# Kernel tuning notes

Hardware: AMD Instinct MI355X
Metric: run time of the kernel (lower is better)

The kernel has to match this reference:

```python
import jax, jax.numpy as jnp
import numpy as np

N = 100_000   # atoms
B = 10_000    # building blocks
E = 320_000   # edges (bb <- atom)
D = 256       # embed_dim
H = 8         # heads
HD = D // H   # head_dim = 32
DIST = 64     # gaussian dist embed dim
MAX_R = 10.0


def setup_inputs() -> dict:
    key = jax.random.key(0)
    ks = jax.random.split(key, 10)
    atom_feats = jax.random.normal(ks[0], (N, D), jnp.float32)
    coords = jax.random.normal(ks[1], (N, 3), jnp.float32) * 3.0
    bb_vec = jnp.sort(jax.random.randint(ks[2], (N,), 0, B, jnp.int32))
    src = jax.random.randint(ks[3], (E,), 0, N, jnp.int32)
    tgt = jax.random.randint(ks[4], (E,), 0, B, jnp.int32)
    # linear params, [in, out] layout (x @ W + b)
    Wq = jax.random.normal(ks[5], (D, D), jnp.float32) / np.sqrt(D)
    Wk = jax.random.normal(ks[6], (D + DIST, D), jnp.float32) / np.sqrt(D + DIST)
    Wv = jax.random.normal(ks[7], (D + DIST, D), jnp.float32) / np.sqrt(D + DIST)
    Wo = jax.random.normal(ks[8], (D, D), jnp.float32) / np.sqrt(D)
    bq = jnp.zeros((D,), jnp.float32)
    bk = jnp.zeros((D,), jnp.float32)
    bv = jnp.zeros((D,), jnp.float32)
    bo = jnp.zeros((D,), jnp.float32)
    return dict(atom_feats=atom_feats, coords=coords, Wq=Wq, bq=bq, Wk=Wk, bk=bk,
                Wv=Wv, bv=bv, Wo=Wo, bo=bo, bb_vec=bb_vec, src=src, tgt=tgt)


def _gaussian_smearing(dist):
    offsets = jnp.linspace(0.0, MAX_R, DIST)            # [DIST]
    coeff = -0.5 / (offsets[1] - offsets[0]) ** 2
    return jnp.exp(coeff * (dist[:, None] - offsets) ** 2)  # [E, DIST]


def reference(atom_feats, coords, Wq, bq, Wk, bk, Wv, bv, Wo, bo, bb_vec, src, tgt):
    # building-block centers: mean coords, summed feats per bb
    counts = jax.ops.segment_sum(jnp.ones((N,), coords.dtype), bb_vec, num_segments=B)
    bb_center_pos = jax.ops.segment_sum(coords, bb_vec, num_segments=B)
    bb_center_pos = bb_center_pos / jnp.maximum(counts, 1.0)[:, None]       # [B, 3]
    bb_center_feats = jax.ops.segment_sum(atom_feats, bb_vec, num_segments=B)  # [B, D]

    # per-edge distance embedding
    edge_vec = coords[src] - bb_center_pos[tgt]                             # [E, 3]
    dist = jnp.sqrt(jnp.sum(edge_vec * edge_vec, axis=-1))                  # [E]
    edge_dist_embed = _gaussian_smearing(dist)                              # [E, DIST]

    # QKV
    q = (bb_center_feats @ Wq + bq).reshape(B, H, HD)                       # [B, H, HD]
    atom_input = jnp.concatenate([atom_feats[src], edge_dist_embed], -1)    # [E, D+DIST]
    k = (atom_input @ Wk + bk).reshape(E, H, HD)
    v = (atom_input @ Wv + bv).reshape(E, H, HD)

    # per-edge attention logits + segment softmax over tgt
    attn = jnp.einsum('ehc,ehc->eh', q[tgt], k) / np.sqrt(HD)               # [E, H]
    seg_max = jax.ops.segment_max(attn, tgt, num_segments=B)                # [B, H]
    ex = jnp.exp(attn - seg_max[tgt])
    denom = jax.ops.segment_sum(ex, tgt, num_segments=B)                    # [B, H]
    attn = ex / (denom[tgt] + 1e-16)

    # weighted scatter-sum of messages
    msg = attn[..., None] * v                                               # [E, H, HD]
    out = jax.ops.segment_sum(msg, tgt, num_segments=B).reshape(B, D)       # [B, D]
    return out @ Wo + bo
```

## Files before the change

### kernel.cpp

```cpp
#include <hip/hip_runtime.h>
#include <math.h>

#define N_ATOMS 100000
#define B_BB    10000
#define E_EDGES 320000
#define D_DIM   256
#define NHEAD   8
#define NDIST   64
#define EPAD    128

#define DELTA   (10.0f/63.0f)
#define GCOEFF  (-0.5f/(DELTA*DELTA))
#define QKSCALE 0.17677669529663687f

__global__ void k_offsets(const int* __restrict__ bb_vec, int* __restrict__ atom_off,
                          int* __restrict__ edge_cnt) {
  int b = blockIdx.x * 256 + threadIdx.x;
  if (b <= B_BB) {
    int lo = 0, hi = N_ATOMS;
    while (lo < hi) { int mid = (lo + hi) >> 1; if (bb_vec[mid] < b) lo = mid + 1; else hi = mid; }
    atom_off[b] = lo;
  }
  if (b < B_BB) edge_cnt[b] = 0;
}

__global__ __launch_bounds__(256) void k_bb_centers(
    const float* __restrict__ af, const float* __restrict__ coords,
    const int* __restrict__ atom_off, float* __restrict__ bbF, float* __restrict__ bb_pos) {
  int t = threadIdx.x;
  for (int b = blockIdx.x; b < B_BB; b += gridDim.x) {
    int s = atom_off[b], e = atom_off[b + 1];
    float acc = 0.f;
    for (int a = s; a < e; a++) acc += af[(size_t)a * D_DIM + t];
    bbF[(size_t)b * D_DIM + t] = acc;
    if (t < 3) {
      float c = 0.f;
      for (int a = s; a < e; a++) c += coords[(size_t)a * 3 + t];
      float cnt = (float)(e - s);
      bb_pos[b * 4 + t] = c / fmaxf(cnt, 1.0f);
    }
  }
}

__global__ __launch_bounds__(256) void k_gemm256(
    const float* __restrict__ A, const float* __restrict__ W,
    const float* __restrict__ bias, float* __restrict__ C, int M) {
  __shared__ __align__(16) float As[16][68];
  __shared__ __align__(16) float Ws[16][64];
  int tid = threadIdx.x;
  int tx = tid & 15, ty = tid >> 4;
  int row0 = blockIdx.x * 64, col0 = blockIdx.y * 64;
  float acc[4][4] = {};
  for (int k0 = 0; k0 < 256; k0 += 16) {
    {
      int r = tid >> 2;
      int c = (tid & 3) * 4;
      int row = row0 + r;
      float4 v = make_float4(0.f, 0.f, 0.f, 0.f);
      if (row < M) v = *(const float4*)&A[(size_t)row * 256 + k0 + c];
      As[c + 0][r] = v.x; As[c + 1][r] = v.y; As[c + 2][r] = v.z; As[c + 3][r] = v.w;
    }
    {
      int r = tid >> 4;
      int c = (tid & 15) * 4;
      float4 v = *(const float4*)&W[(size_t)(k0 + r) * 256 + col0 + c];
      *(float4*)&Ws[r][c] = v;
    }
    __syncthreads();
#pragma unroll
    for (int kk = 0; kk < 16; kk++) {
      float4 a = *(const float4*)&As[kk][ty * 4];
      float4 b = *(const float4*)&Ws[kk][tx * 4];
      float av[4] = {a.x, a.y, a.z, a.w};
      float bv4[4] = {b.x, b.y, b.z, b.w};
#pragma unroll
      for (int i = 0; i < 4; i++)
#pragma unroll
        for (int j = 0; j < 4; j++) acc[i][j] += av[i] * bv4[j];
    }
    __syncthreads();
  }
#pragma unroll
  for (int i = 0; i < 4; i++) {
    int row = row0 + ty * 4 + i;
    if (row < M) {
      int col = col0 + tx * 4;
      float4 r = make_float4(acc[i][0] + bias[col + 0], acc[i][1] + bias[col + 1],
                             acc[i][2] + bias[col + 2], acc[i][3] + bias[col + 3]);
      *(float4*)&C[(size_t)row * 256 + col] = r;
    }
  }
}

__global__ void k_hist(const int* __restrict__ tgt, int* __restrict__ edge_cnt) {
  int e = blockIdx.x * 256 + threadIdx.x;
  if (e < E_EDGES) atomicAdd(&edge_cnt[tgt[e]], 1);
}

__global__ __launch_bounds__(1024) void k_scan(
    const int* __restrict__ edge_cnt, int* __restrict__ edge_start, int* __restrict__ cursor,
    int* __restrict__ src_sorted, float* __restrict__ dist_sorted) {
  __shared__ int ssum[1024];
  int tid = threadIdx.x;
  int base = tid * 10;
  int v[10]; int s = 0;
#pragma unroll
  for (int k = 0; k < 10; k++) { int i = base + k; v[k] = (i < B_BB) ? edge_cnt[i] : 0; s += v[k]; }
  ssum[tid] = s;
  __syncthreads();
  for (int off = 1; off < 1024; off <<= 1) {
    int t = (tid >= off) ? ssum[tid - off] : 0;
    __syncthreads();
    ssum[tid] += t;
    __syncthreads();
  }
  int excl = ssum[tid] - s;
#pragma unroll
  for (int k = 0; k < 10; k++) {
    int i = base + k;
    if (i < B_BB) { edge_start[i] = excl; cursor[i] = excl; }
    excl += v[k];
  }
  if (tid == 1023) edge_start[B_BB] = E_EDGES;
  if (tid < EPAD) { src_sorted[E_EDGES + tid] = 0; dist_sorted[E_EDGES + tid] = 0.f; }
}

__global__ void k_fill(const int* __restrict__ src, const int* __restrict__ tgt,
                       const float* __restrict__ coords, const float* __restrict__ bb_pos,
                       int* __restrict__ cursor, int* __restrict__ src_sorted,
                       float* __restrict__ dist_sorted) {
  int e = blockIdx.x * 256 + threadIdx.x;
  if (e >= E_EDGES) return;
  int b = tgt[e], a = src[e];
  int pos = atomicAdd(&cursor[b], 1);
  float dx = coords[a * 3 + 0] - bb_pos[b * 4 + 0];
  float dy = coords[a * 3 + 1] - bb_pos[b * 4 + 1];
  float dz = coords[a * 3 + 2] - bb_pos[b * 4 + 2];
  src_sorted[pos] = a;
  dist_sorted[pos] = sqrtf(dx * dx + dy * dy + dz * dz);
}

__global__ __launch_bounds__(256) void k_wt(
    const float* __restrict__ q, const float* __restrict__ Wk, float* __restrict__ wt) {
  __shared__ __align__(16) float As[32][132];
  __shared__ __align__(16) float Bs[32][68];
  int tid = threadIdx.x;
  int b0 = blockIdx.x * 128;
  int i0 = blockIdx.y * 64;
  int h  = blockIdx.z;
  {
    int r = tid >> 1, c0 = (tid & 1) * 16;
    int row = b0 + r;
    const float* qp = q + (size_t)row * 256 + h * 32 + c0;
#pragma unroll
    for (int jj = 0; jj < 4; ++jj) {
      float4 v = make_float4(0.f, 0.f, 0.f, 0.f);
      if (row < B_BB) v = *(const float4*)(qp + 4 * jj);
      As[c0 + 4*jj + 0][r] = v.x; As[c0 + 4*jj + 1][r] = v.y;
      As[c0 + 4*jj + 2][r] = v.z; As[c0 + 4*jj + 3][r] = v.w;
    }
  }
  {
    int r = tid >> 2, c0 = (tid & 3) * 8;
    const float* wp = Wk + (size_t)(i0 + r) * 256 + h * 32 + c0;
#pragma unroll
    for (int jj = 0; jj < 2; ++jj) {
      float4 v = *(const float4*)(wp + 4 * jj);
      Bs[c0 + 4*jj + 0][r] = v.x; Bs[c0 + 4*jj + 1][r] = v.y;
      Bs[c0 + 4*jj + 2][r] = v.z; Bs[c0 + 4*jj + 3][r] = v.w;
    }
  }
  __syncthreads();
  int tx = tid & 15, ty = tid >> 4;
  float acc[8][4] = {};
#pragma unroll
  for (int kk = 0; kk < 32; ++kk) {
    float4 a0 = *(const float4*)&As[kk][ty * 8];
    float4 a1 = *(const float4*)&As[kk][ty * 8 + 4];
    float4 b4 = *(const float4*)&Bs[kk][tx * 4];
    float av[8] = {a0.x, a0.y, a0.z, a0.w, a1.x, a1.y, a1.z, a1.w};
    float bv4[4] = {b4.x, b4.y, b4.z, b4.w};
#pragma unroll
    for (int i = 0; i < 8; ++i)
#pragma unroll
      for (int j = 0; j < 4; ++j) acc[i][j] += av[i] * bv4[j];
  }
#pragma unroll
  for (int i = 0; i < 8; ++i) {
    int row = b0 + ty * 8 + i;
    if (row < B_BB) {
      float4 o = make_float4(acc[i][0] * QKSCALE, acc[i][1] * QKSCALE,
                             acc[i][2] * QKSCALE, acc[i][3] * QKSCALE);
      *(float4*)&wt[(size_t)row * 2560 + h * 320 + i0 + tx * 4] = o;
    }
  }
}

#define FMA4(p, v, Wb, k) \
  p = fmaf((v).x, Wb[(k)], p);   p = fmaf((v).y, Wb[(k)+1], p); \
  p = fmaf((v).z, Wb[(k)+2], p); p = fmaf((v).w, Wb[(k)+3], p);

#define ACC4(Sarr, k, ww, v) \
  Sarr[(k)]   = fmaf(ww, (v).x, Sarr[(k)]);   Sarr[(k)+1] = fmaf(ww, (v).y, Sarr[(k)+1]); \
  Sarr[(k)+2] = fmaf(ww, (v).z, Sarr[(k)+2]); Sarr[(k)+3] = fmaf(ww, (v).w, Sarr[(k)+3]);

__global__ __launch_bounds__(256) void k_attn(
    const float* __restrict__ af, float* __restrict__ wtS,
    const int* __restrict__ edge_start, const int* __restrict__ src_sorted,
    const float* __restrict__ dist_sorted, float* __restrict__ wsum) {
  int tid = threadIdx.x;
  int lane = tid & 63;
  int wv = tid >> 6;
  int h0 = 2 * wv, h1 = 2 * wv + 1;
  int g = lane >> 4;
  int sub = lane & 15;
  int b = blockIdx.x;

  int s0 = edge_start[b], e1 = edge_start[b + 1];
  float* wtb = wtS + (size_t)b * 2560;
  const float* wr0 = wtb + h0 * 320;
  const float* wr1 = wtb + h1 * 320;

  float W0[16], W1[16], wd0[4], wd1[4];
#pragma unroll
  for (int j = 0; j < 4; ++j) {
    float4 t0 = *(const float4*)(wr0 + sub * 16 + 4 * j);
    float4 t1 = *(const float4*)(wr1 + sub * 16 + 4 * j);
    W0[4*j+0] = t0.x; W0[4*j+1] = t0.y; W0[4*j+2] = t0.z; W0[4*j+3] = t0.w;
    W1[4*j+0] = t1.x; W1[4*j+1] = t1.y; W1[4*j+2] = t1.z; W1[4*j+3] = t1.w;
  }
#pragma unroll
  for (int j = 0; j < 4; ++j) { wd0[j] = wr0[256 + sub + 16*j]; wd1[j] = wr1[256 + sub + 16*j]; }

  float cj[4];
#pragma unroll
  for (int j = 0; j < 4; ++j) cj[j] = (float)(sub + 16 * j) * DELTA;

  float l0 = 0.f, l1 = 0.f;
  float S0r[16] = {}, S1r[16] = {};
  float sd0[4] = {}, sd1[4] = {};

  if (s0 < e1) {
    int iaC = src_sorted[s0 + 8 + g];
    int iaD = src_sorted[s0 + 12 + g];
    float ddA = dist_sorted[s0 + g];
    float ddB = dist_sorted[s0 + 4 + g];
    float ddC = dist_sorted[s0 + 8 + g];
    float ddD = dist_sorted[s0 + 12 + g];
    int iaA = src_sorted[s0 + g];
    int iaB = src_sorted[s0 + 4 + g];
    const float4* rA = (const float4*)(af + (size_t)iaA * 256 + sub * 16);
    const float4* rB = (const float4*)(af + (size_t)iaB * 256 + sub * 16);
    float4 A0 = rA[0], A1 = rA[1], A2 = rA[2], A3 = rA[3];
    float4 B0 = rB[0], B1 = rB[1], B2 = rB[2], B3 = rB[3];

    for (int eb = s0; eb < e1; eb += 8) {
      int iaC2 = src_sorted[eb + 16 + g];
      float ddC2 = dist_sorted[eb + 16 + g];
      int iaD2 = src_sorted[eb + 20 + g];
      float ddD2 = dist_sorted[eb + 20 + g];
      const float4* rC = (const float4*)(af + (size_t)iaC * 256 + sub * 16);
      float4 C0 = rC[0], C1 = rC[1], C2 = rC[2], C3 = rC[3];

      float embA[4], embB[4];
#pragma unroll
      for (int j = 0; j < 4; ++j) {
        float da = ddA - cj[j]; embA[j] = __expf(GCOEFF * da * da);
        float db = ddB - cj[j]; embB[j] = __expf(GCOEFF * db * db);
      }
      float pA0 = 0.f, pA1 = 0.f, pB0 = 0.f, pB1 = 0.f;
      FMA4(pA0, A0, W0, 0);  FMA4(pA1, A0, W1, 0);
      FMA4(pB0, B0, W0, 0);  FMA4(pB1, B0, W1, 0);
      FMA4(pA0, A1, W0, 4);  FMA4(pA1, A1, W1, 4);
      FMA4(pB0, B1, W0, 4);  FMA4(pB1, B1, W1, 4);
      FMA4(pA0, A2, W0, 8);  FMA4(pA1, A2, W1, 8);
      FMA4(pB0, B2, W0, 8);  FMA4(pB1, B2, W1, 8);
      FMA4(pA0, A3, W0, 12); FMA4(pA1, A3, W1, 12);
      FMA4(pB0, B3, W0, 12); FMA4(pB1, B3, W1, 12);
#pragma unroll
      for (int j = 0; j < 4; ++j) {
        pA0 = fmaf(embA[j], wd0[j], pA0); pA1 = fmaf(embA[j], wd1[j], pA1);
        pB0 = fmaf(embB[j], wd0[j], pB0); pB1 = fmaf(embB[j], wd1[j], pB1);
      }
#pragma unroll
      for (int off = 8; off > 0; off >>= 1) {
        pA0 += __shfl_xor(pA0, off);
        pA1 += __shfl_xor(pA1, off);
        pB0 += __shfl_xor(pB0, off);
        pB1 += __shfl_xor(pB1, off);
      }
      float wA0 = __expf(pA0), wA1 = __expf(pA1);
      float wB0 = __expf(pB0), wB1 = __expf(pB1);
      if (eb + g >= e1)     { wA0 = 0.f; wA1 = 0.f; }
      if (eb + 4 + g >= e1) { wB0 = 0.f; wB1 = 0.f; }
      l0 += wA0 + wB0; l1 += wA1 + wB1;
#pragma unroll
      for (int j = 0; j < 4; ++j) {
        sd0[j] = fmaf(wA0, embA[j], sd0[j]); sd1[j] = fmaf(wA1, embA[j], sd1[j]);
        sd0[j] = fmaf(wB0, embB[j], sd0[j]); sd1[j] = fmaf(wB1, embB[j], sd1[j]);
      }

      ACC4(S0r, 0,  wA0, A0); ACC4(S1r, 0,  wA1, A0);
      ACC4(S0r, 4,  wA0, A1); ACC4(S1r, 4,  wA1, A1);
      ACC4(S0r, 8,  wA0, A2); ACC4(S1r, 8,  wA1, A2);
      ACC4(S0r, 12, wA0, A3); ACC4(S1r, 12, wA1, A3);

      const float4* rD = (const float4*)(af + (size_t)iaD * 256 + sub * 16);
      float4 D0 = rD[0], D1 = rD[1], D2 = rD[2], D3 = rD[3];

      ACC4(S0r, 0,  wB0, B0); ACC4(S1r, 0,  wB1, B0);
      ACC4(S0r, 4,  wB0, B1); ACC4(S1r, 4,  wB1, B1);
      ACC4(S0r, 8,  wB0, B2); ACC4(S1r, 8,  wB1, B2);
      ACC4(S0r, 12, wB0, B3); ACC4(S1r, 12, wB1, B3);

      A0 = C0; A1 = C1; A2 = C2; A3 = C3;
      B0 = D0; B1 = D1; B2 = D2; B3 = D3;
      ddA = ddC; ddB = ddD; ddC = ddC2; ddD = ddD2;
      iaC = iaC2; iaD = iaD2;
    }
  }

#pragma unroll
  for (int off = 16; off <= 32; off <<= 1) {
    l0 += __shfl_xor(l0, off);
    l1 += __shfl_xor(l1, off);
#pragma unroll
    for (int c = 0; c < 16; ++c) {
      S0r[c] += __shfl_xor(S0r[c], off);
      S1r[c] += __shfl_xor(S1r[c], off);
    }
#pragma unroll
    for (int j = 0; j < 4; ++j) {
      sd0[j] += __shfl_xor(sd0[j], off);
      sd1[j] += __shfl_xor(sd1[j], off);
    }
  }

  float inv0 = 1.0f / (l0 + 1e-16f), inv1 = 1.0f / (l1 + 1e-16f);
  if (g == 0) {
#pragma unroll
    for (int j = 0; j < 4; ++j) {
      float4 o0 = make_float4(S0r[4*j+0]*inv0, S0r[4*j+1]*inv0, S0r[4*j+2]*inv0, S0r[4*j+3]*inv0);
      float4 o1 = make_float4(S1r[4*j+0]*inv1, S1r[4*j+1]*inv1, S1r[4*j+2]*inv1, S1r[4*j+3]*inv1);
      *(float4*)(wtb + h0 * 320 + sub * 16 + 4 * j) = o0;
      *(float4*)(wtb + h1 * 320 + sub * 16 + 4 * j) = o1;
    }
#pragma unroll
    for (int j = 0; j < 4; ++j) {
      wtb[h0 * 320 + 256 + sub + 16 * j] = sd0[j] * inv0;
      wtb[h1 * 320 + 256 + sub + 16 * j] = sd1[j] * inv1;
    }
    if (sub == 0) {
      wsum[b * 8 + h0] = l0 * inv0;
      wsum[b * 8 + h1] = l1 * inv1;
    }
  }
}

__global__ __launch_bounds__(256) void k_out_head(
    const float* __restrict__ Sf, const float* __restrict__ Wv,
    const float* __restrict__ bv, const float* __restrict__ wsum,
    float* __restrict__ out_pre) {
  __shared__ __align__(16) float As[32][132];
  __shared__ __align__(16) float Bs[32][36];
  int tid = threadIdx.x;
  int b0 = blockIdx.x * 128;
  int h  = blockIdx.y;
  int tx = tid & 7, ty = tid >> 3;
  float acc[4][4] = {};
  for (int k0 = 0; k0 < 320; k0 += 32) {
    {
      int r = tid >> 1, c0 = (tid & 1) * 16;
      int row = b0 + r;
      const float* sp = Sf + (size_t)row * 2560 + h * 320 + k0 + c0;
#pragma unroll
      for (int jj = 0; jj < 4; ++jj) {
        float4 v = make_float4(0.f, 0.f, 0.f, 0.f);
        if (row < B_BB) v = *(const float4*)(sp + 4 * jj);
        As[c0 + 4*jj + 0][r] = v.x; As[c0 + 4*jj + 1][r] = v.y;
        As[c0 + 4*jj + 2][r] = v.z; As[c0 + 4*jj + 3][r] = v.w;
      }
    }
    {
      int r = tid >> 3, c0 = (tid & 7) * 4;
      float4 v = *(const float4*)&Wv[(size_t)(k0 + r) * 256 + h * 32 + c0];
      *(float4*)&Bs[r][c0] = v;
    }
    __syncthreads();
#pragma unroll
    for (int kk = 0; kk < 32; ++kk) {
      float4 a4 = *(const float4*)&As[kk][ty * 4];
      float4 b4 = *(const float4*)&Bs[kk][tx * 4];
      float av[4] = {a4.x, a4.y, a4.z, a4.w};
      float bv4[4] = {b4.x, b4.y, b4.z, b4.w};
#pragma unroll
      for (int i = 0; i < 4; ++i)
#pragma unroll
        for (int j = 0; j < 4; ++j) acc[i][j] += av[i] * bv4[j];
    }
    __syncthreads();
  }
  float bvv[4];
#pragma unroll
  for (int j = 0; j < 4; ++j) bvv[j] = bv[h * 32 + tx * 4 + j];
#pragma unroll
  for (int i = 0; i < 4; ++i) {
    int row = b0 + ty * 4 + i;
    if (row < B_BB) {
      float ws = wsum[row * 8 + h];
      float4 o = make_float4(acc[i][0] + ws * bvv[0], acc[i][1] + ws * bvv[1],
                             acc[i][2] + ws * bvv[2], acc[i][3] + ws * bvv[3]);
      *(float4*)&out_pre[(size_t)row * 256 + h * 32 + tx * 4] = o;
    }
  }
}

extern "C" void kernel_launch(void* const* d_in, const int* in_sizes, int n_in,
                              void* d_out, int out_size, void* d_ws, size_t ws_size,
                              hipStream_t stream) {
  const float* af     = (const float*)d_in[0];
  const float* coords = (const float*)d_in[1];
  const float* Wq     = (const float*)d_in[2];
  const float* bq     = (const float*)d_in[3];
  const float* Wk     = (const float*)d_in[4];
  const float* bk     = (const float*)d_in[5];  (void)bk;
  const float* Wv     = (const float*)d_in[6];
  const float* bv     = (const float*)d_in[7];
  const float* Wo     = (const float*)d_in[8];
  const float* bo     = (const float*)d_in[9];
  const int* bb_vec   = (const int*)d_in[10];
  const int* src      = (const int*)d_in[11];
  const int* tgt      = (const int*)d_in[12];
  float* out = (float*)d_out;
  (void)in_sizes; (void)n_in; (void)out_size; (void)ws_size;

  char* ws = (char*)d_ws;
  size_t o = 0;
  auto alloc = [&](size_t bytes) { size_t r = o; o += (bytes + 255) & ~(size_t)255; return r; };
  int*   atom_off    = (int*)(ws + alloc((B_BB + 1) * 4));
  int*   edge_cnt    = (int*)(ws + alloc((size_t)B_BB * 4));
  int*   edge_start  = (int*)(ws + alloc((B_BB + 1) * 4));
  int*   cursor      = (int*)(ws + alloc((size_t)B_BB * 4));
  int*   src_sorted  = (int*)(ws + alloc((size_t)(E_EDGES + EPAD) * 4));
  float* dist_sorted = (float*)(ws + alloc((size_t)(E_EDGES + EPAD) * 4));
  float* bbF         = (float*)(ws + alloc((size_t)B_BB * 256 * 4));
  float* bb_pos      = (float*)(ws + alloc((size_t)B_BB * 4 * 4));
  float* q           = (float*)(ws + alloc((size_t)B_BB * 256 * 4));
  float* wtS         = (float*)(ws + alloc((size_t)B_BB * 2560 * 4));
  float* wsum        = (float*)(ws + alloc((size_t)B_BB * 8 * 4));
  float* out_pre     = (float*)(ws + alloc((size_t)B_BB * 256 * 4));

  k_offsets<<<(B_BB + 1 + 255) / 256, 256, 0, stream>>>(bb_vec, atom_off, edge_cnt);
  k_bb_centers<<<2560, 256, 0, stream>>>(af, coords, atom_off, bbF, bb_pos);
  k_hist<<<(E_EDGES + 255) / 256, 256, 0, stream>>>(tgt, edge_cnt);
  k_scan<<<1, 1024, 0, stream>>>(edge_cnt, edge_start, cursor, src_sorted, dist_sorted);
  k_fill<<<(E_EDGES + 255) / 256, 256, 0, stream>>>(src, tgt, coords, bb_pos, cursor,
                                                    src_sorted, dist_sorted);
  k_gemm256<<<dim3((B_BB + 63) / 64, 4), 256, 0, stream>>>(bbF, Wq, bq, q, B_BB);
  k_wt<<<dim3((B_BB + 127) / 128, 5, 8), 256, 0, stream>>>(q, Wk, wtS);
  k_attn<<<B_BB, 256, 0, stream>>>(af, wtS, edge_start, src_sorted, dist_sorted, wsum);
  k_out_head<<<dim3((B_BB + 127) / 128, 8), 256, 0, stream>>>(wtS, Wv, bv, wsum, out_pre);
  k_gemm256<<<dim3((B_BB + 63) / 64, 4), 256, 0, stream>>>(out_pre, Wo, bo, out, B_BB);
}
```

Baseline: 557.7 us.

## Double-buffer shared tiles in gemm256 and process several blocks per attention workgroup

The 256-wide GEMM now uses ping-pong shared-memory tiles. The next K-slice is loaded into registers while the current slice is computed, which removes one barrier per iteration and hides global load latency. The attention kernel now loops over four building blocks per workgroup instead of launching one workgroup per block. This cuts launch and scheduling overhead but reduces the grid to 2500 workgroups, which can leave more load imbalance across CUs since per-block edge counts vary.

```diff
diff --git a/kernel.cpp b/kernel.cpp
--- a/kernel.cpp
+++ b/kernel.cpp
@@ -8,6 +8,7 @@
 #define NHEAD   8
 #define NDIST   64
 #define EPAD    128
+#define BB_PER_BLK 4
 
 #define DELTA   (10.0f/63.0f)
 #define GCOEFF  (-0.5f/(DELTA*DELTA))
@@ -45,32 +46,38 @@
 __global__ __launch_bounds__(256) void k_gemm256(
     const float* __restrict__ A, const float* __restrict__ W,
     const float* __restrict__ bias, float* __restrict__ C, int M) {
-  __shared__ __align__(16) float As[16][68];
-  __shared__ __align__(16) float Ws[16][64];
+  __shared__ __align__(16) float As[2][16][68];
+  __shared__ __align__(16) float Ws[2][16][64];
   int tid = threadIdx.x;
   int tx = tid & 15, ty = tid >> 4;
   int row0 = blockIdx.x * 64, col0 = blockIdx.y * 64;
+  int ar = tid >> 2, ac = (tid & 3) * 4;
+  int wr = tid >> 4, wc = (tid & 15) * 4;
+  int arow = row0 + ar;
+  const float* Ap = A + (size_t)arow * 256 + ac;
+  const float* Wp = W + (size_t)wr * 256 + col0 + wc;
   float acc[4][4] = {};
+  {
+    float4 va = make_float4(0.f, 0.f, 0.f, 0.f);
+    if (arow < M) va = *(const float4*)Ap;
+    As[0][ac + 0][ar] = va.x; As[0][ac + 1][ar] = va.y;
+    As[0][ac + 2][ar] = va.z; As[0][ac + 3][ar] = va.w;
+    *(float4*)&Ws[0][wr][wc] = *(const float4*)Wp;
+  }
+  __syncthreads();
+  int cur = 0;
   for (int k0 = 0; k0 < 256; k0 += 16) {
-    {
-      int r = tid >> 2;
-      int c = (tid & 3) * 4;
-      int row = row0 + r;
-      float4 v = make_float4(0.f, 0.f, 0.f, 0.f);
-      if (row < M) v = *(const float4*)&A[(size_t)row * 256 + k0 + c];
-      As[c + 0][r] = v.x; As[c + 1][r] = v.y; As[c + 2][r] = v.z; As[c + 3][r] = v.w;
-    }
-    {
-      int r = tid >> 4;
-      int c = (tid & 15) * 4;
-      float4 v = *(const float4*)&W[(size_t)(k0 + r) * 256 + col0 + c];
-      *(float4*)&Ws[r][c] = v;
-    }
-    __syncthreads();
+    float4 va, vw;
+    bool nxt = (k0 + 16) < 256;
+    if (nxt) {
+      va = make_float4(0.f, 0.f, 0.f, 0.f);
+      if (arow < M) va = *(const float4*)(Ap + k0 + 16);
+      vw = *(const float4*)(Wp + (size_t)(k0 + 16) * 256);
+    }
 #pragma unroll
     for (int kk = 0; kk < 16; kk++) {
-      float4 a = *(const float4*)&As[kk][ty * 4];
-      float4 b = *(const float4*)&Ws[kk][tx * 4];
+      float4 a = *(const float4*)&As[cur][kk][ty * 4];
+      float4 b = *(const float4*)&Ws[cur][kk][tx * 4];
       float av[4] = {a.x, a.y, a.z, a.w};
       float bv4[4] = {b.x, b.y, b.z, b.w};
 #pragma unroll
@@ -78,7 +85,13 @@
 #pragma unroll
         for (int j = 0; j < 4; j++) acc[i][j] += av[i] * bv4[j];
     }
-    __syncthreads();
+    if (nxt) {
+      As[cur ^ 1][ac + 0][ar] = va.x; As[cur ^ 1][ac + 1][ar] = va.y;
+      As[cur ^ 1][ac + 2][ar] = va.z; As[cur ^ 1][ac + 3][ar] = va.w;
+      *(float4*)&Ws[cur ^ 1][wr][wc] = vw;
+      __syncthreads();
+      cur ^= 1;
+    }
   }
 #pragma unroll
   for (int i = 0; i < 4; i++) {
@@ -214,145 +227,149 @@
   int h0 = 2 * wv, h1 = 2 * wv + 1;
   int g = lane >> 4;
   int sub = lane & 15;
-  int b = blockIdx.x;
-
-  int s0 = edge_start[b], e1 = edge_start[b + 1];
-  float* wtb = wtS + (size_t)b * 2560;
-  const float* wr0 = wtb + h0 * 320;
-  const float* wr1 = wtb + h1 * 320;
-
-  float W0[16], W1[16], wd0[4], wd1[4];
-#pragma unroll
-  for (int j = 0; j < 4; ++j) {
-    float4 t0 = *(const float4*)(wr0 + sub * 16 + 4 * j);
-    float4 t1 = *(const float4*)(wr1 + sub * 16 + 4 * j);
-    W0[4*j+0] = t0.x; W0[4*j+1] = t0.y; W0[4*j+2] = t0.z; W0[4*j+3] = t0.w;
-    W1[4*j+0] = t1.x; W1[4*j+1] = t1.y; W1[4*j+2] = t1.z; W1[4*j+3] = t1.w;
-  }
-#pragma unroll
-  for (int j = 0; j < 4; ++j) { wd0[j] = wr0[256 + sub + 16*j]; wd1[j] = wr1[256 + sub + 16*j]; }
 
   float cj[4];
 #pragma unroll
   for (int j = 0; j < 4; ++j) cj[j] = (float)(sub + 16 * j) * DELTA;
 
-  float l0 = 0.f, l1 = 0.f;
-  float S0r[16] = {}, S1r[16] = {};
-  float sd0[4] = {}, sd1[4] = {};
-
-  if (s0 < e1) {
-    int iaC = src_sorted[s0 + 8 + g];
-    int iaD = src_sorted[s0 + 12 + g];
-    float ddA = dist_sorted[s0 + g];
-    float ddB = dist_sorted[s0 + 4 + g];
-    float ddC = dist_sorted[s0 + 8 + g];
-    float ddD = dist_sorted[s0 + 12 + g];
-    int iaA = src_sorted[s0 + g];
-    int iaB = src_sorted[s0 + 4 + g];
-    const float4* rA = (const float4*)(af + (size_t)iaA * 256 + sub * 16);
-    const float4* rB = (const float4*)(af + (size_t)iaB * 256 + sub * 16);
-    float4 A0 = rA[0], A1 = rA[1], A2 = rA[2], A3 = rA[3];
-    float4 B0 = rB[0], B1 = rB[1], B2 = rB[2], B3 = rB[3];
-
-    for (int eb = s0; eb < e1; eb += 8) {
-      int iaC2 = src_sorted[eb + 16 + g];
-      float ddC2 = dist_sorted[eb + 16 + g];
-      int iaD2 = src_sorted[eb + 20 + g];
-      float ddD2 = dist_sorted[eb + 20 + g];
-      const float4* rC = (const float4*)(af + (size_t)iaC * 256 + sub * 16);
-      float4 C0 = rC[0], C1 = rC[1], C2 = rC[2], C3 = rC[3];
-
-      float embA[4], embB[4];
+  for (int bi = 0; bi < BB_PER_BLK; ++bi) {
+    int b = blockIdx.x * BB_PER_BLK + bi;
+    if (b >= B_BB) break;
+
+    int s0 = edge_start[b], e1 = edge_start[b + 1];
+    float* wtb = wtS + (size_t)b * 2560;
+    const float* wr0 = wtb + h0 * 320;
+    const float* wr1 = wtb + h1 * 320;
+
+    float W0[16], W1[16], wd0[4], wd1[4];
+#pragma unroll
+    for (int j = 0; j < 4; ++j) {
+      float4 t0 = *(const float4*)(wr0 + sub * 16 + 4 * j);
+      float4 t1 = *(const float4*)(wr1 + sub * 16 + 4 * j);
+      W0[4*j+0] = t0.x; W0[4*j+1] = t0.y; W0[4*j+2] = t0.z; W0[4*j+3] = t0.w;
+      W1[4*j+0] = t1.x; W1[4*j+1] = t1.y; W1[4*j+2] = t1.z; W1[4*j+3] = t1.w;
+    }
+#pragma unroll
+    for (int j = 0; j < 4; ++j) { wd0[j] = wr0[256 + sub + 16*j]; wd1[j] = wr1[256 + sub + 16*j]; }
+
+    float l0 = 0.f, l1 = 0.f;
+    float S0r[16] = {}, S1r[16] = {};
+    float sd0[4] = {}, sd1[4] = {};
+
+    if (s0 < e1) {
+      int iaC = src_sorted[s0 + 8 + g];
+      int iaD = src_sorted[s0 + 12 + g];
+      float ddA = dist_sorted[s0 + g];
+      float ddB = dist_sorted[s0 + 4 + g];
+      float ddC = dist_sorted[s0 + 8 + g];
+      float ddD = dist_sorted[s0 + 12 + g];
+      int iaA = src_sorted[s0 + g];
+      int iaB = src_sorted[s0 + 4 + g];
+      const float4* rA = (const float4*)(af + (size_t)iaA * 256 + sub * 16);
+      const float4* rB = (const float4*)(af + (size_t)iaB * 256 + sub * 16);
+      float4 A0 = rA[0], A1 = rA[1], A2 = rA[2], A3 = rA[3];
+      float4 B0 = rB[0], B1 = rB[1], B2 = rB[2], B3 = rB[3];
+
+      for (int eb = s0; eb < e1; eb += 8) {
+        int iaC2 = src_sorted[eb + 16 + g];
+        float ddC2 = dist_sorted[eb + 16 + g];
+        int iaD2 = src_sorted[eb + 20 + g];
+        float ddD2 = dist_sorted[eb + 20 + g];
+        const float4* rC = (const float4*)(af + (size_t)iaC * 256 + sub * 16);
+        float4 C0 = rC[0], C1 = rC[1], C2 = rC[2], C3 = rC[3];
+
+        float embA[4], embB[4];
+#pragma unroll
+        for (int j = 0; j < 4; ++j) {
+          float da = ddA - cj[j]; embA[j] = __expf(GCOEFF * da * da);
+          float db = ddB - cj[j]; embB[j] = __expf(GCOEFF * db * db);
+        }
+        float pA0 = 0.f, pA1 = 0.f, pB0 = 0.f, pB1 = 0.f;
+        FMA4(pA0, A0, W0, 0);  FMA4(pA1, A0, W1, 0);
+        FMA4(pB0, B0, W0, 0);  FMA4(pB1, B0, W1, 0);
+        FMA4(pA0, A1, W0, 4);  FMA4(pA1, A1, W1, 4);
+        FMA4(pB0, B1, W0, 4);  FMA4(pB1, B1, W1, 4);
+        FMA4(pA0, A2, W0, 8);  FMA4(pA1, A2, W1, 8);
+        FMA4(pB0, B2, W0, 8);  FMA4(pB1, B2, W1, 8);
+        FMA4(pA0, A3, W0, 12); FMA4(pA1, A3, W1, 12);
+        FMA4(pB0, B3, W0, 12); FMA4(pB1, B3, W1, 12);
+#pragma unroll
+        for (int j = 0; j < 4; ++j) {
+          pA0 = fmaf(embA[j], wd0[j], pA0); pA1 = fmaf(embA[j], wd1[j], pA1);
+          pB0 = fmaf(embB[j], wd0[j], pB0); pB1 = fmaf(embB[j], wd1[j], pB1);
+        }
+#pragma unroll
+        for (int off = 8; off > 0; off >>= 1) {
+          pA0 += __shfl_xor(pA0, off);
+          pA1 += __shfl_xor(pA1, off);
+          pB0 += __shfl_xor(pB0, off);
+          pB1 += __shfl_xor(pB1, off);
+        }
+        float wA0 = __expf(pA0), wA1 = __expf(pA1);
+        float wB0 = __expf(pB0), wB1 = __expf(pB1);
+        if (eb + g >= e1)     { wA0 = 0.f; wA1 = 0.f; }
+        if (eb + 4 + g >= e1) { wB0 = 0.f; wB1 = 0.f; }
+        l0 += wA0 + wB0; l1 += wA1 + wB1;
+#pragma unroll
+        for (int j = 0; j < 4; ++j) {
+          sd0[j] = fmaf(wA0, embA[j], sd0[j]); sd1[j] = fmaf(wA1, embA[j], sd1[j]);
+          sd0[j] = fmaf(wB0, embB[j], sd0[j]); sd1[j] = fmaf(wB1, embB[j], sd1[j]);
+        }
+
+        ACC4(S0r, 0,  wA0, A0); ACC4(S1r, 0,  wA1, A0);
+        ACC4(S0r, 4,  wA0, A1); ACC4(S1r, 4,  wA1, A1);
+        ACC4(S0r, 8,  wA0, A2); ACC4(S1r, 8,  wA1, A2);
+        ACC4(S0r, 12, wA0, A3); ACC4(S1r, 12, wA1, A3);
+
+        const float4* rD = (const float4*)(af + (size_t)iaD * 256 + sub * 16);
+        float4 D0 = rD[0], D1 = rD[1], D2 = rD[2], D3 = rD[3];
+
+        ACC4(S0r, 0,  wB0, B0); ACC4(S1r, 0,  wB1, B0);
+        ACC4(S0r, 4,  wB0, B1); ACC4(S1r, 4,  wB1, B1);
+        ACC4(S0r, 8,  wB0, B2); ACC4(S1r, 8,  wB1, B2);
+        ACC4(S0r, 12, wB0, B3); ACC4(S1r, 12, wB1, B3);
+
+        A0 = C0; A1 = C1; A2 = C2; A3 = C3;
+        B0 = D0; B1 = D1; B2 = D2; B3 = D3;
+        ddA = ddC; ddB = ddD; ddC = ddC2; ddD = ddD2;
+        iaC = iaC2; iaD = iaD2;
+      }
+    }
+
+#pragma unroll
+    for (int off = 16; off <= 32; off <<= 1) {
+      l0 += __shfl_xor(l0, off);
+      l1 += __shfl_xor(l1, off);
+#pragma unroll
+      for (int c = 0; c < 16; ++c) {
+        S0r[c] += __shfl_xor(S0r[c], off);
+        S1r[c] += __shfl_xor(S1r[c], off);
+      }
 #pragma unroll
       for (int j = 0; j < 4; ++j) {
-        float da = ddA - cj[j]; embA[j] = __expf(GCOEFF * da * da);
-        float db = ddB - cj[j]; embB[j] = __expf(GCOEFF * db * db);
-      }
-      float pA0 = 0.f, pA1 = 0.f, pB0 = 0.f, pB1 = 0.f;
-      FMA4(pA0, A0, W0, 0);  FMA4(pA1, A0, W1, 0);
-      FMA4(pB0, B0, W0, 0);  FMA4(pB1, B0, W1, 0);
-      FMA4(pA0, A1, W0, 4);  FMA4(pA1, A1, W1, 4);
-      FMA4(pB0, B1, W0, 4);  FMA4(pB1, B1, W1, 4);
-      FMA4(pA0, A2, W0, 8);  FMA4(pA1, A2, W1, 8);
-      FMA4(pB0, B2, W0, 8);  FMA4(pB1, B2, W1, 8);
-      FMA4(pA0, A3, W0, 12); FMA4(pA1, A3, W1, 12);
-      FMA4(pB0, B3, W0, 12); FMA4(pB1, B3, W1, 12);
+        sd0[j] += __shfl_xor(sd0[j], off);
+        sd1[j] += __shfl_xor(sd1[j], off);
+      }
+    }
+
+    float inv0 = 1.0f / (l0 + 1e-16f), inv1 = 1.0f / (l1 + 1e-16f);
+    if (g == 0) {
 #pragma unroll
       for (int j = 0; j < 4; ++j) {
-        pA0 = fmaf(embA[j], wd0[j], pA0); pA1 = fmaf(embA[j], wd1[j], pA1);
-        pB0 = fmaf(embB[j], wd0[j], pB0); pB1 = fmaf(embB[j], wd1[j], pB1);
-      }
-#pragma unroll
-      for (int off = 8; off > 0; off >>= 1) {
-        pA0 += __shfl_xor(pA0, off);
-        pA1 += __shfl_xor(pA1, off);
-        pB0 += __shfl_xor(pB0, off);
-        pB1 += __shfl_xor(pB1, off);
-      }
-      float wA0 = __expf(pA0), wA1 = __expf(pA1);
-      float wB0 = __expf(pB0), wB1 = __expf(pB1);
-      if (eb + g >= e1)     { wA0 = 0.f; wA1 = 0.f; }
-      if (eb + 4 + g >= e1) { wB0 = 0.f; wB1 = 0.f; }
-      l0 += wA0 + wB0; l1 += wA1 + wB1;
+        float4 o0 = make_float4(S0r[4*j+0]*inv0, S0r[4*j+1]*inv0, S0r[4*j+2]*inv0, S0r[4*j+3]*inv0);
+        float4 o1 = make_float4(S1r[4*j+0]*inv1, S1r[4*j+1]*inv1, S1r[4*j+2]*inv1, S1r[4*j+3]*inv1);
+        *(float4*)(wtb + h0 * 320 + sub * 16 + 4 * j) = o0;
+        *(float4*)(wtb + h1 * 320 + sub * 16 + 4 * j) = o1;
+      }
 #pragma unroll
       for (int j = 0; j < 4; ++j) {
-        sd0[j] = fmaf(wA0, embA[j], sd0[j]); sd1[j] = fmaf(wA1, embA[j], sd1[j]);
-        sd0[j] = fmaf(wB0, embB[j], sd0[j]); sd1[j] = fmaf(wB1, embB[j], sd1[j]);
-      }
-
-      ACC4(S0r, 0,  wA0, A0); ACC4(S1r, 0,  wA1, A0);
-      ACC4(S0r, 4,  wA0, A1); ACC4(S1r, 4,  wA1, A1);
-      ACC4(S0r, 8,  wA0, A2); ACC4(S1r, 8,  wA1, A2);
-      ACC4(S0r, 12, wA0, A3); ACC4(S1r, 12, wA1, A3);
-
-      const float4* rD = (const float4*)(af + (size_t)iaD * 256 + sub * 16);
-      float4 D0 = rD[0], D1 = rD[1], D2 = rD[2], D3 = rD[3];
-
-      ACC4(S0r, 0,  wB0, B0); ACC4(S1r, 0,  wB1, B0);
-      ACC4(S0r, 4,  wB0, B1); ACC4(S1r, 4,  wB1, B1);
-      ACC4(S0r, 8,  wB0, B2); ACC4(S1r, 8,  wB1, B2);
-      ACC4(S0r, 12, wB0, B3); ACC4(S1r, 12, wB1, B3);
-
-      A0 = C0; A1 = C1; A2 = C2; A3 = C3;
-      B0 = D0; B1 = D1; B2 = D2; B3 = D3;
-      ddA = ddC; ddB = ddD; ddC = ddC2; ddD = ddD2;
-      iaC = iaC2; iaD = iaD2;
-    }
-  }
-
-#pragma unroll
-  for (int off = 16; off <= 32; off <<= 1) {
-    l0 += __shfl_xor(l0, off);
-    l1 += __shfl_xor(l1, off);
-#pragma unroll
-    for (int c = 0; c < 16; ++c) {
-      S0r[c] += __shfl_xor(S0r[c], off);
-      S1r[c] += __shfl_xor(S1r[c], off);
-    }
-#pragma unroll
-    for (int j = 0; j < 4; ++j) {
-      sd0[j] += __shfl_xor(sd0[j], off);
-      sd1[j] += __shfl_xor(sd1[j], off);
-    }
-  }
-
-  float inv0 = 1.0f / (l0 + 1e-16f), inv1 = 1.0f / (l1 + 1e-16f);
-  if (g == 0) {
-#pragma unroll
-    for (int j = 0; j < 4; ++j) {
-      float4 o0 = make_float4(S0r[4*j+0]*inv0, S0r[4*j+1]*inv0, S0r[4*j+2]*inv0, S0r[4*j+3]*inv0);
-      float4 o1 = make_float4(S1r[4*j+0]*inv1, S1r[4*j+1]*inv1, S1r[4*j+2]*inv1, S1r[4*j+3]*inv1);
-      *(float4*)(wtb + h0 * 320 + sub * 16 + 4 * j) = o0;
-      *(float4*)(wtb + h1 * 320 + sub * 16 + 4 * j) = o1;
-    }
-#pragma unroll
-    for (int j = 0; j < 4; ++j) {
-      wtb[h0 * 320 + 256 + sub + 16 * j] = sd0[j] * inv0;
-      wtb[h1 * 320 + 256 + sub + 16 * j] = sd1[j] * inv1;
-    }
-    if (sub == 0) {
-      wsum[b * 8 + h0] = l0 * inv0;
-      wsum[b * 8 + h1] = l1 * inv1;
+        wtb[h0 * 320 + 256 + sub + 16 * j] = sd0[j] * inv0;
+        wtb[h1 * 320 + 256 + sub + 16 * j] = sd1[j] * inv1;
+      }
+      if (sub == 0) {
+        wsum[b * 8 + h0] = l0 * inv0;
+        wsum[b * 8 + h1] = l1 * inv1;
+      }
     }
   }
 }
@@ -458,7 +475,8 @@
                                                     src_sorted, dist_sorted);
   k_gemm256<<<dim3((B_BB + 63) / 64, 4), 256, 0, stream>>>(bbF, Wq, bq, q, B_BB);
   k_wt<<<dim3((B_BB + 127) / 128, 5, 8), 256, 0, stream>>>(q, Wk, wtS);
-  k_attn<<<B_BB, 256, 0, stream>>>(af, wtS, edge_start, src_sorted, dist_sorted, wsum);
+  k_attn<<<(B_BB + BB_PER_BLK - 1) / BB_PER_BLK, 256, 0, stream>>>(
+      af, wtS, edge_start, src_sorted, dist_sorted, wsum);
   k_out_head<<<dim3((B_BB + 127) / 128, 8), 256, 0, stream>>>(wtS, Wv, bv, wsum, out_pre);
   k_gemm256<<<dim3((B_BB + 63) / 64, 4), 256, 0, stream>>>(out_pre, Wo, bo, out, B_BB);
 }
```

Measured after the change: 559.2 us. About the same (+0.3%).
